# Kernel tuning notes

Measured on AMD Instinct MI355X. Metric: run time of the kernel, lower is better.

## Reference

```python
import jax, jax.numpy as jnp
import numpy as np

N_IN, IN_DIM, N_OUT, OUT_DIM, N_ROUTING = 1152, 8, 10, 16, 3


def squash(x, axis=-1):
    norm = jnp.linalg.norm(x, axis=axis, keepdims=True)
    norm2 = norm * norm
    scale = norm2 / (1.0 + norm2) / norm
    return scale * x


def setup_inputs() -> dict:
    key = jax.random.key(0)
    k1, k2 = jax.random.split(key)
    u = jax.random.normal(k1, (256, N_IN, IN_DIM), dtype=jnp.float32)
    # kaiming-uniform-ish init for W [nInCaps, inCapsDim, nOutCaps*outCapsDim]
    fan_in = IN_DIM
    bound = float(np.sqrt(6.0 / fan_in))
    W = jax.random.uniform(k2, (N_IN, IN_DIM, N_OUT * OUT_DIM), dtype=jnp.float32,
                           minval=-bound, maxval=bound)
    return {"u": u, "W": W}


def reference(u, W):
    B = u.shape[0]
    # uhat[b,n,m] = sum_i u[b,n,i] * W[n,i,m]
    uhat = jnp.einsum('bni,nim->bnm', u, W)
    uhat = uhat.reshape(B, N_IN, N_OUT, OUT_DIM)
    uhat_d = jax.lax.stop_gradient(uhat)  # detach=True

    b = jnp.zeros((B, N_IN, N_OUT), dtype=u.dtype)
    v = None
    for i in range(N_ROUTING):
        c = jax.nn.softmax(b, axis=-1)[..., None]        # [B, nIn, nOut, 1]
        src = uhat if i == N_ROUTING - 1 else uhat_d
        s = jnp.sum(c * src, axis=1)                     # [B, nOut, outDim]
        v = squash(s)
        if i != N_ROUTING - 1:
            a = jnp.sum(uhat_d * v[:, None], axis=-1)    # [B, nIn, nOut]
            b = b + a
    return v
```

## Files before the change

kernel.cpp:

```cpp
#include <hip/hip_runtime.h>
#include <math.h>

#define B    256
#define NIN  1152
#define IND  8
#define NOUT 10
#define OUTD 16
#define M    160
#define K    9216

typedef _Float16 h2    __attribute__((ext_vector_type(2)));
typedef _Float16 f16x4 __attribute__((ext_vector_type(4)));
typedef _Float16 f16x8 __attribute__((ext_vector_type(8)));
typedef float    f32x4 __attribute__((ext_vector_type(4)));
struct __align__(16) H8 { h2 h[4]; };
struct __align__(8)  H4 { h2 h[2]; };

__global__ __launch_bounds__(256) void k_w16(const float* __restrict__ W,
                                             _Float16* __restrict__ Wh) {
    const int t = blockIdx.x * 256 + threadIdx.x;
    const float4 f = *(const float4*)(W + (size_t)t * 4);
    H4 p;
    p.h[0] = h2{(_Float16)f.x, (_Float16)f.y};
    p.h[1] = h2{(_Float16)f.z, (_Float16)f.w};
    *(H4*)(Wh + (size_t)t * 4) = p;
}

__global__ __launch_bounds__(256) void k_u16(const float* __restrict__ u,
                                             _Float16* __restrict__ u16) {
    const size_t t = (size_t)blockIdx.x * 256 + threadIdx.x;
    const float4 f = *(const float4*)(u + t * 4);
    H4 p;
    p.h[0] = h2{(_Float16)f.x, (_Float16)f.y};
    p.h[1] = h2{(_Float16)f.z, (_Float16)f.w};
    *(H4*)(u16 + t * 4) = p;
}

__global__ __launch_bounds__(256) void k_ut(const float* __restrict__ u,
                                            _Float16* __restrict__ ut) {
    __shared__ _Float16 lt[64][80];
    const int k0 = blockIdx.x * 64;
    const int b0 = blockIdx.y * 64;
#pragma unroll
    for (int p = 0; p < 4; ++p) {
        const int r = (threadIdx.x >> 4) + p * 16;
        const int c = (threadIdx.x & 15) * 4;
        const float4 f = *(const float4*)(u + (size_t)(b0 + r) * K + k0 + c);
        lt[c + 0][r] = (_Float16)f.x;
        lt[c + 1][r] = (_Float16)f.y;
        lt[c + 2][r] = (_Float16)f.z;
        lt[c + 3][r] = (_Float16)f.w;
    }
    __syncthreads();
#pragma unroll
    for (int p = 0; p < 2; ++p) {
        const int kr = (threadIdx.x >> 3) + p * 32;
        const int bc = (threadIdx.x & 7) * 8;
        *(uint4*)(ut + (size_t)(k0 + kr) * B + b0 + bc) = *(const uint4*)&lt[kr][bc];
    }
}

__global__ __launch_bounds__(256) void k_wt(const float* __restrict__ W,
                                            _Float16* __restrict__ Wt) {
    __shared__ float wl[IND * M];
    const int n = blockIdx.x;
    const float* src = W + (size_t)n * IND * M;
    for (int t = threadIdx.x; t < IND * M / 4; t += 256)
        *(float4*)(wl + t * 4) = *(const float4*)(src + (size_t)t * 4);
    __syncthreads();
    const int t = threadIdx.x;
    if (t < 160) {
        const int o = t >> 4, d = t & 15;
        f16x8 out;
#pragma unroll
        for (int i = 0; i < IND; ++i) out[i] = (_Float16)wl[i * M + o * OUTD + d];
        *(f16x8*)(Wt + (((size_t)n * NOUT + o) * OUTD + d) * IND) = out;
    }
}

#define NSPLIT 96
#define GPS    3

template <int MODE>
__global__ __launch_bounds__(128, 4) void k_su(const _Float16* __restrict__ u16,
                                               const _Float16* __restrict__ Wt,
                                               const _Float16* __restrict__ cbuf,
                                               _Float16* __restrict__ spart) {
    const int lane  = threadIdx.x & 63;
    const int wv    = threadIdx.x >> 6;
    const int btile = blockIdx.x;
    const int split = blockIdx.y;
    const int bl    = lane & 15;
    const int q     = lane >> 4;
    const int b     = btile * 16 + bl;
    const int nbase = split * (GPS * 4);

    f32x4 acc[5];
#pragma unroll
    for (int j = 0; j < 5; ++j) acc[j] = f32x4{0.f, 0.f, 0.f, 0.f};

#pragma unroll
    for (int g = 0; g < GPS; ++g) {
        const int n = nbase + g * 4 + q;
        const f16x8 uf = *(const f16x8*)(u16 + ((size_t)b * NIN + n) * IND);
#pragma unroll
        for (int j = 0; j < 5; ++j) {
            const int o = wv * 5 + j;
            f16x8 a;
            if (MODE) {
                const _Float16 cv = cbuf[((size_t)o * NIN + n) * B + b];
#pragma unroll
                for (int i = 0; i < IND; ++i) a[i] = uf[i] * cv;
            } else {
                a = uf;
            }
            const f16x8 bf =
                *(const f16x8*)(Wt + (((size_t)n * NOUT + o) * OUTD + bl) * IND);
            acc[j] = __builtin_amdgcn_mfma_f32_16x16x32_f16(a, bf, acc[j], 0, 0, 0);
        }
    }

    const float scale = MODE ? 1.0f : 0.1f;
    _Float16* sp = spart + (size_t)split * B * M + ((size_t)btile * 16) * M;
#pragma unroll
    for (int r = 0; r < 4; ++r) {
        const int brow = q * 4 + r;
#pragma unroll
        for (int j = 0; j < 5; ++j) {
            const int o = wv * 5 + j;
            sp[(size_t)brow * M + o * OUTD + bl] = (_Float16)(acc[j][r] * scale);
        }
    }
}

template <int OUT16>
__global__ __launch_bounds__(64) void k_squash(const _Float16* __restrict__ spart,
                                               void* __restrict__ dstv) {
    const int gid = blockIdx.x * 64 + threadIdx.x;
    float s = 0.f;
#pragma unroll 16
    for (int ch = 0; ch < NSPLIT; ++ch) s += (float)spart[(size_t)ch * B * M + gid];
    float ss = s * s;
    ss += __shfl_xor(ss, 1);
    ss += __shfl_xor(ss, 2);
    ss += __shfl_xor(ss, 4);
    ss += __shfl_xor(ss, 8);
    const float v = s * sqrtf(ss) / (1.f + ss);
    if (OUT16) {
        const int b = gid / M, m = gid % M, o = m >> 4, d = m & 15;
        ((_Float16*)dstv)[((size_t)o * B + b) * 16 + d] = (_Float16)v;
    } else {
        ((float*)dstv)[gid] = v;
    }
}

#define NPW  4

template <int FIRST>
__global__ __launch_bounds__(256, 8) void k_a(const _Float16* __restrict__ ut,
                                              const _Float16* __restrict__ Wh,
                                              const _Float16* __restrict__ vt,
                                              _Float16* __restrict__ blog,
                                              _Float16* __restrict__ cbuf) {
    const int lane = threadIdx.x & 63;
    const int wv   = threadIdx.x >> 6;
    const int np   = blockIdx.x * NPW + wv;
    const int col  = lane & 15;
    const int q    = lane >> 4;
    const int b0   = blockIdx.y * 16;
    const int b    = b0 + col;
    const int nl   = col >> 3, ii = col & 7;
    const int nout = np * 2 + (q >> 1);

    float uf[4];
    {
        const _Float16* up = ut + ((size_t)np * 16 + q * 4) * B + b;
#pragma unroll
        for (int r = 0; r < 4; ++r) uf[r] = (float)up[(size_t)r * B];
    }

    const _Float16* wa = Wh + (((size_t)np * 2 + nl) * IND + ii) * M + q * 4;
    const f32x4 zero = {0.f, 0.f, 0.f, 0.f};

    float areg[NOUT];
#pragma unroll
    for (int o = 0; o < NOUT; ++o) {
        const f16x4 af = *(const f16x4*)(wa + o * OUTD);
        const f16x4 bfr = *(const f16x4*)(vt + ((size_t)o * B + b) * 16 + q * 4);
        const f32x4 cp = __builtin_amdgcn_mfma_f32_16x16x16f16(af, bfr, zero, 0, 0, 0);
        float s = cp[0] * uf[0];
        s = fmaf(cp[1], uf[1], s);
        s = fmaf(cp[2], uf[2], s);
        s = fmaf(cp[3], uf[3], s);
        s += __shfl_xor(s, 16);
        areg[o] = s;
    }

    float bl[NOUT];
    _Float16* bp = blog + ((size_t)nout * NOUT) * B + b;
    if (FIRST) {
#pragma unroll
        for (int o = 0; o < NOUT; ++o) {
            bl[o] = areg[o];
            if ((q & 1) == 0) bp[(size_t)o * B] = (_Float16)bl[o];
        }
    } else {
#pragma unroll
        for (int o = 0; o < NOUT; ++o) bl[o] = (float)bp[(size_t)o * B] + areg[o];
    }
    float mx = bl[0];
#pragma unroll
    for (int o = 1; o < NOUT; ++o) mx = fmaxf(mx, bl[o]);
    float sum = 0.f;
#pragma unroll
    for (int o = 0; o < NOUT; ++o) { bl[o] = __expf(bl[o] - mx); sum += bl[o]; }
    const float inv = 1.f / sum;
    if ((q & 1) == 0) {
#pragma unroll
        for (int o = 0; o < NOUT; ++o)
            cbuf[((size_t)o * NIN + nout) * B + b] = (_Float16)(bl[o] * inv);
    }
}

extern "C" void kernel_launch(void* const* d_in, const int* in_sizes, int n_in,
                              void* d_out, int out_size, void* d_ws, size_t ws_size,
                              hipStream_t stream) {
    const float* u = (const float*)d_in[0];
    const float* W = (const float*)d_in[1];
    float* out = (float*)d_out;

    char* ws = (char*)d_ws;
    _Float16* spart = (_Float16*)(ws);
    _Float16* blog  = (_Float16*)(ws + 7864320);
    _Float16* cbuf  = (_Float16*)(ws + 13762560);
    _Float16* vt    = (_Float16*)(ws + 19660800);
    _Float16* Wh    = (_Float16*)(ws + 19742720);
    _Float16* Wt    = (_Float16*)(ws + 22691840);
    _Float16* u16   = (_Float16*)(ws + 25640960);
    _Float16* ut    = (_Float16*)(ws + 30359552);

    const dim3 gs(16, NSPLIT);
    const dim3 ga(NIN / 2 / NPW, B / 16);

    k_w16<<<1440, 256, 0, stream>>>(W, Wh);
    k_wt<<<NIN, 256, 0, stream>>>(W, Wt);
    k_u16<<<2304, 256, 0, stream>>>(u, u16);
    k_ut<<<dim3(K / 64, B / 64), 256, 0, stream>>>(u, ut);

    k_su<0><<<gs, 128, 0, stream>>>(u16, Wt, cbuf, spart);
    k_squash<1><<<640, 64, 0, stream>>>(spart, vt);
    k_a<1><<<ga, 256, 0, stream>>>(ut, Wh, vt, blog, cbuf);
    k_su<1><<<gs, 128, 0, stream>>>(u16, Wt, cbuf, spart);
    k_squash<1><<<640, 64, 0, stream>>>(spart, vt);
    k_a<0><<<ga, 256, 0, stream>>>(ut, Wh, vt, blog, cbuf);
    k_su<1><<<gs, 128, 0, stream>>>(u16, Wt, cbuf, spart);
    k_squash<0><<<640, 64, 0, stream>>>(spart, out);
}
```

Measured before the change: 89.77 us.

## Fuse input conversion kernels and halve split-K partials with in-block reduction

Merges the four fp16 preparation kernels into two, so W and u are each read once while producing both layouts. The s=sum(c*uhat) kernel now uses 256-thread blocks in which two wave pairs each take half of a larger n-range and combine their results through shared memory. This halves the number of split partials (96 to 48), which cuts partial-sum writes and the squash reduction reads. The cost is a __syncthreads, some LDS traffic, and a squash kernel with fewer, larger blocks.

```diff
diff --git a/kernel.cpp b/kernel.cpp
--- a/kernel.cpp
+++ b/kernel.cpp
@@ -16,78 +16,71 @@
 struct __align__(16) H8 { h2 h[4]; };
 struct __align__(8)  H4 { h2 h[2]; };
 
-__global__ __launch_bounds__(256) void k_w16(const float* __restrict__ W,
-                                             _Float16* __restrict__ Wh) {
-    const int t = blockIdx.x * 256 + threadIdx.x;
-    const float4 f = *(const float4*)(W + (size_t)t * 4);
-    H4 p;
-    p.h[0] = h2{(_Float16)f.x, (_Float16)f.y};
-    p.h[1] = h2{(_Float16)f.z, (_Float16)f.w};
-    *(H4*)(Wh + (size_t)t * 4) = p;
-}
-
-__global__ __launch_bounds__(256) void k_u16(const float* __restrict__ u,
-                                             _Float16* __restrict__ u16) {
-    const size_t t = (size_t)blockIdx.x * 256 + threadIdx.x;
-    const float4 f = *(const float4*)(u + t * 4);
-    H4 p;
-    p.h[0] = h2{(_Float16)f.x, (_Float16)f.y};
-    p.h[1] = h2{(_Float16)f.z, (_Float16)f.w};
-    *(H4*)(u16 + t * 4) = p;
-}
-
-__global__ __launch_bounds__(256) void k_ut(const float* __restrict__ u,
-                                            _Float16* __restrict__ ut) {
-    __shared__ _Float16 lt[64][80];
-    const int k0 = blockIdx.x * 64;
-    const int b0 = blockIdx.y * 64;
-#pragma unroll
-    for (int p = 0; p < 4; ++p) {
-        const int r = (threadIdx.x >> 4) + p * 16;
-        const int c = (threadIdx.x & 15) * 4;
-        const float4 f = *(const float4*)(u + (size_t)(b0 + r) * K + k0 + c);
-        lt[c + 0][r] = (_Float16)f.x;
-        lt[c + 1][r] = (_Float16)f.y;
-        lt[c + 2][r] = (_Float16)f.z;
-        lt[c + 3][r] = (_Float16)f.w;
-    }
-    __syncthreads();
-#pragma unroll
-    for (int p = 0; p < 2; ++p) {
-        const int kr = (threadIdx.x >> 3) + p * 32;
-        const int bc = (threadIdx.x & 7) * 8;
-        *(uint4*)(ut + (size_t)(k0 + kr) * B + b0 + bc) = *(const uint4*)&lt[kr][bc];
-    }
-}
-
-__global__ __launch_bounds__(256) void k_wt(const float* __restrict__ W,
-                                            _Float16* __restrict__ Wt) {
+__global__ __launch_bounds__(256) void k_prep_w(const float* __restrict__ W,
+                                                _Float16* __restrict__ Wh,
+                                                _Float16* __restrict__ Wt) {
     __shared__ float wl[IND * M];
     const int n = blockIdx.x;
     const float* src = W + (size_t)n * IND * M;
     for (int t = threadIdx.x; t < IND * M / 4; t += 256)
         *(float4*)(wl + t * 4) = *(const float4*)(src + (size_t)t * 4);
     __syncthreads();
-    const int t = threadIdx.x;
-    if (t < 160) {
-        const int o = t >> 4, d = t & 15;
-        f16x8 out;
-#pragma unroll
-        for (int i = 0; i < IND; ++i) out[i] = (_Float16)wl[i * M + o * OUTD + d];
-        *(f16x8*)(Wt + (((size_t)n * NOUT + o) * OUTD + d) * IND) = out;
-    }
-}
-
-#define NSPLIT 96
-#define GPS    3
+    _Float16* wh = Wh + (size_t)n * IND * M;
+    for (int t = threadIdx.x; t < IND * M / 2; t += 256) {
+        h2 p = {(_Float16)wl[2 * t], (_Float16)wl[2 * t + 1]};
+        *(h2*)(wh + 2 * t) = p;
+    }
+    if (threadIdx.x < 160) {
+        const int o = threadIdx.x >> 4, d = threadIdx.x & 15;
+        f16x8 outv;
+#pragma unroll
+        for (int i = 0; i < IND; ++i) outv[i] = (_Float16)wl[i * M + o * OUTD + d];
+        *(f16x8*)(Wt + (((size_t)n * NOUT + o) * OUTD + d) * IND) = outv;
+    }
+}
+
+__global__ __launch_bounds__(256) void k_prep_u(const float* __restrict__ u,
+                                                _Float16* __restrict__ u16,
+                                                _Float16* __restrict__ ut) {
+    __shared__ _Float16 lt[64][80];
+    const int k0 = blockIdx.x * 64;
+    const int b0 = blockIdx.y * 64;
+#pragma unroll
+    for (int p = 0; p < 4; ++p) {
+        const int r = (threadIdx.x >> 4) + p * 16;
+        const int c = (threadIdx.x & 15) * 4;
+        const float4 f = *(const float4*)(u + (size_t)(b0 + r) * K + k0 + c);
+        H4 pk;
+        pk.h[0] = h2{(_Float16)f.x, (_Float16)f.y};
+        pk.h[1] = h2{(_Float16)f.z, (_Float16)f.w};
+        *(H4*)(u16 + (size_t)(b0 + r) * K + k0 + c) = pk;
+        lt[c + 0][r] = (_Float16)f.x;
+        lt[c + 1][r] = (_Float16)f.y;
+        lt[c + 2][r] = (_Float16)f.z;
+        lt[c + 3][r] = (_Float16)f.w;
+    }
+    __syncthreads();
+#pragma unroll
+    for (int p = 0; p < 2; ++p) {
+        const int kr = (threadIdx.x >> 3) + p * 32;
+        const int bc = (threadIdx.x & 7) * 8;
+        *(uint4*)(ut + (size_t)(k0 + kr) * B + b0 + bc) = *(const uint4*)&lt[kr][bc];
+    }
+}
+
+#define NSPLIT 48
+#define GPS    6
 
 template <int MODE>
-__global__ __launch_bounds__(128, 4) void k_su(const _Float16* __restrict__ u16,
+__global__ __launch_bounds__(256, 8) void k_su(const _Float16* __restrict__ u16,
                                                const _Float16* __restrict__ Wt,
                                                const _Float16* __restrict__ cbuf,
                                                _Float16* __restrict__ spart) {
+    __shared__ f32x4 red[2][5][64];
     const int lane  = threadIdx.x & 63;
-    const int wv    = threadIdx.x >> 6;
+    const int w     = threadIdx.x >> 6;
+    const int wp    = w & 1;
+    const int gh    = w >> 1;
     const int btile = blockIdx.x;
     const int split = blockIdx.y;
     const int bl    = lane & 15;
@@ -100,12 +93,13 @@
     for (int j = 0; j < 5; ++j) acc[j] = f32x4{0.f, 0.f, 0.f, 0.f};
 
 #pragma unroll
-    for (int g = 0; g < GPS; ++g) {
+    for (int gg = 0; gg < 3; ++gg) {
+        const int g = gh * 3 + gg;
         const int n = nbase + g * 4 + q;
         const f16x8 uf = *(const f16x8*)(u16 + ((size_t)b * NIN + n) * IND);
 #pragma unroll
         for (int j = 0; j < 5; ++j) {
-            const int o = wv * 5 + j;
+            const int o = wp * 5 + j;
             f16x8 a;
             if (MODE) {
                 const _Float16 cv = cbuf[((size_t)o * NIN + n) * B + b];
@@ -120,23 +114,32 @@
         }
     }
 
-    const float scale = MODE ? 1.0f : 0.1f;
-    _Float16* sp = spart + (size_t)split * B * M + ((size_t)btile * 16) * M;
-#pragma unroll
-    for (int r = 0; r < 4; ++r) {
-        const int brow = q * 4 + r;
+    if (gh == 1) {
+#pragma unroll
+        for (int j = 0; j < 5; ++j) red[wp][j][lane] = acc[j];
+    }
+    __syncthreads();
+    if (gh == 0) {
+        const float scale = MODE ? 1.0f : 0.1f;
+        _Float16* sp = spart + (size_t)split * B * M + ((size_t)btile * 16) * M;
 #pragma unroll
         for (int j = 0; j < 5; ++j) {
-            const int o = wv * 5 + j;
-            sp[(size_t)brow * M + o * OUTD + bl] = (_Float16)(acc[j][r] * scale);
+            const f32x4 other = red[wp][j][lane];
+            const int o = wp * 5 + j;
+#pragma unroll
+            for (int r = 0; r < 4; ++r) {
+                const int brow = q * 4 + r;
+                sp[(size_t)brow * M + o * OUTD + bl] =
+                    (_Float16)((acc[j][r] + other[r]) * scale);
+            }
         }
     }
 }
 
 template <int OUT16>
-__global__ __launch_bounds__(64) void k_squash(const _Float16* __restrict__ spart,
-                                               void* __restrict__ dstv) {
-    const int gid = blockIdx.x * 64 + threadIdx.x;
+__global__ __launch_bounds__(256) void k_squash(const _Float16* __restrict__ spart,
+                                                void* __restrict__ dstv) {
+    const int gid = blockIdx.x * 256 + threadIdx.x;
     float s = 0.f;
 #pragma unroll 16
     for (int ch = 0; ch < NSPLIT; ++ch) s += (float)spart[(size_t)ch * B * M + gid];
@@ -231,28 +234,26 @@
 
     char* ws = (char*)d_ws;
     _Float16* spart = (_Float16*)(ws);
-    _Float16* blog  = (_Float16*)(ws + 7864320);
-    _Float16* cbuf  = (_Float16*)(ws + 13762560);
-    _Float16* vt    = (_Float16*)(ws + 19660800);
-    _Float16* Wh    = (_Float16*)(ws + 19742720);
-    _Float16* Wt    = (_Float16*)(ws + 22691840);
-    _Float16* u16   = (_Float16*)(ws + 25640960);
-    _Float16* ut    = (_Float16*)(ws + 30359552);
+    _Float16* blog  = (_Float16*)(ws + 3932160);
+    _Float16* cbuf  = (_Float16*)(ws + 9830400);
+    _Float16* vt    = (_Float16*)(ws + 15728640);
+    _Float16* Wh    = (_Float16*)(ws + 15810560);
+    _Float16* Wt    = (_Float16*)(ws + 18759680);
+    _Float16* ut    = (_Float16*)(ws + 21708800);
+    _Float16* u16   = (_Float16*)(ws + 26427392);
 
     const dim3 gs(16, NSPLIT);
     const dim3 ga(NIN / 2 / NPW, B / 16);
 
-    k_w16<<<1440, 256, 0, stream>>>(W, Wh);
-    k_wt<<<NIN, 256, 0, stream>>>(W, Wt);
-    k_u16<<<2304, 256, 0, stream>>>(u, u16);
-    k_ut<<<dim3(K / 64, B / 64), 256, 0, stream>>>(u, ut);
-
-    k_su<0><<<gs, 128, 0, stream>>>(u16, Wt, cbuf, spart);
-    k_squash<1><<<640, 64, 0, stream>>>(spart, vt);
+    k_prep_w<<<NIN, 256, 0, stream>>>(W, Wh, Wt);
+    k_prep_u<<<dim3(K / 64, B / 64), 256, 0, stream>>>(u, u16, ut);
+
+    k_su<0><<<gs, 256, 0, stream>>>(u16, Wt, cbuf, spart);
+    k_squash<1><<<160, 256, 0, stream>>>(spart, vt);
     k_a<1><<<ga, 256, 0, stream>>>(ut, Wh, vt, blog, cbuf);
-    k_su<1><<<gs, 128, 0, stream>>>(u16, Wt, cbuf, spart);
-    k_squash<1><<<640, 64, 0, stream>>>(spart, vt);
+    k_su<1><<<gs, 256, 0, stream>>>(u16, Wt, cbuf, spart);
+    k_squash<1><<<160, 256, 0, stream>>>(spart, vt);
     k_a<0><<<ga, 256, 0, stream>>>(ut, Wh, vt, blog, cbuf);
-    k_su<1><<<gs, 128, 0, stream>>>(u16, Wt, cbuf, spart);
-    k_squash<0><<<640, 64, 0, stream>>>(spart, out);
-}
+    k_su<1><<<gs, 256, 0, stream>>>(u16, Wt, cbuf, spart);
+    k_squash<0><<<160, 256, 0, stream>>>(spart, out);
+}
```

After: 77.60 us (median of 2 runs). -13.6%, faster.
